# Kernel optimization log

Hardware: AMD Instinct MI355X
Metric: run time of the kernel (lower is better)

## Reference

```python
import jax, jax.numpy as jnp
import numpy as np

EPS = 1e-5  # torch LayerNorm default

def setup_inputs() -> dict:
    key = jax.random.key(0)
    ks = jax.random.split(key, 4)
    S, B, D, BN = 4096, 8, 1024, 128
    x = jax.random.normal(ks[0], (S, B, D), dtype=jnp.float32)
    residual = jax.random.normal(ks[1], (B, S, D), dtype=jnp.float32)
    # xavier_uniform init for adapter projections
    lim_d = float(np.sqrt(6.0 / (D + BN)))
    W_down = jax.random.uniform(ks[2], (BN, D), minval=-lim_d, maxval=lim_d, dtype=jnp.float32)
    W_up = jax.random.uniform(ks[3], (D, BN), minval=-lim_d, maxval=lim_d, dtype=jnp.float32)
    return {
        "x": x,
        "residual": residual,
        "ln_gamma": jnp.ones((D,), jnp.float32),
        "ln_beta": jnp.zeros((D,), jnp.float32),
        "W_down": W_down,
        "b_down": jnp.zeros((BN,), jnp.float32),
        "W_up": W_up,
        "b_up": jnp.zeros((D,), jnp.float32),
    }

def reference(x, residual, ln_gamma, ln_beta, W_down, b_down, W_up, b_up):
    # ffn_fn is an opaque callable (treated as identity here); x: [S,B,D]
    x = x + jnp.swapaxes(residual, 0, 1)           # residual.transpose(0,1)
    shortcut = x
    # NaiveAdapter: LayerNorm -> down -> ReLU -> up -> residual add
    mu = jnp.mean(x, axis=-1, keepdims=True)
    var = jnp.mean(jnp.square(x - mu), axis=-1, keepdims=True)
    h = (x - mu) * jax.lax.rsqrt(var + EPS) * ln_gamma + ln_beta
    h = jax.nn.relu(jnp.einsum('sbd,kd->sbk', h, W_down) + b_down)  # [S,B,BN]
    h = jnp.einsum('sbk,dk->sbd', h, W_up) + b_up                   # [S,B,D]
    return h + shortcut
```

## Files before the change

kernel.cpp:

```cpp
#include <hip/hip_runtime.h>

#define S_DIM 4096
#define B_DIM 8
#define D_DIM 1024
#define BN_DIM 128
#define M_DIM (S_DIM * B_DIM)
#define LDT 40
#define CLD 132

typedef short s8v __attribute__((ext_vector_type(8)));
typedef float f4v __attribute__((ext_vector_type(4)));

__device__ __forceinline__ unsigned short f2bf(float f) {
  union { unsigned int i; float f; } v; v.f = f;
  unsigned int r = v.i + 0x7FFFu + ((v.i >> 16) & 1u);
  return (unsigned short)(r >> 16);
}
__device__ __forceinline__ float bf2f(unsigned short u) {
  union { unsigned int i; float f; } v; v.i = ((unsigned int)u) << 16; return v.f;
}

__global__ __launch_bounds__(256) void prep_kernel(
    const float* __restrict__ Wd_f, const float* __restrict__ bd_f,
    const float* __restrict__ Wu_f, const float* __restrict__ gamma,
    const float* __restrict__ beta,
    unsigned short* __restrict__ Wd, float* __restrict__ bd,
    unsigned short* __restrict__ Wu) {
  __shared__ float red[4];
  int t = threadIdx.x;
  if (blockIdx.x < 128) {
    int n = blockIdx.x, k = t * 4;
    float4 w = *(const float4*)&Wd_f[n * 1024 + k];
    float4 g = *(const float4*)&gamma[k];
    float4 bt = *(const float4*)&beta[k];
    ushort4 o;
    o.x = f2bf(w.x * g.x); o.y = f2bf(w.y * g.y);
    o.z = f2bf(w.z * g.z); o.w = f2bf(w.w * g.w);
    *(ushort4*)&Wd[n * 1024 + k] = o;
    float bs = w.x * bt.x + w.y * bt.y + w.z * bt.z + w.w * bt.w;
#pragma unroll
    for (int ofs = 32; ofs >= 1; ofs >>= 1) bs += __shfl_xor(bs, ofs, 64);
    if ((t & 63) == 0) red[t >> 6] = bs;
    __syncthreads();
    if (t == 0) bd[n] = bd_f[n] + red[0] + red[1] + red[2] + red[3];
  } else {
    int j = blockIdx.x - 128;
#pragma unroll
    for (int c = 0; c < 4; ++c) {
      int idx = j * 4096 + c * 1024 + t * 4;
      float4 w = *(const float4*)&Wu_f[idx];
      ushort4 o;
      o.x = f2bf(w.x); o.y = f2bf(w.y); o.z = f2bf(w.z); o.w = f2bf(w.w);
      *(ushort4*)&Wu[idx] = o;
    }
    __syncthreads();
  }
}

__global__ __launch_bounds__(256) void add_ln_kernel(
    const float* __restrict__ x, const float* __restrict__ res,
    unsigned short* __restrict__ y, float2* __restrict__ stats) {
  int wave = threadIdx.x >> 6, lane = threadIdx.x & 63;
  int row0 = blockIdx.x * 8 + wave * 2;

  float4 xa[2][4], ra[2][4];
#pragma unroll
  for (int p = 0; p < 2; ++p) {
    int row = row0 + p;
    const float* xr = x + (size_t)row * D_DIM;
    const float* rr = res + ((size_t)(row & 7) * S_DIM + (row >> 3)) * D_DIM;
#pragma unroll
    for (int c = 0; c < 4; ++c) {
      int e = c * 256 + lane * 4;
      xa[p][c] = *(const float4*)&xr[e];
      ra[p][c] = *(const float4*)&rr[e];
    }
  }
  float sum[2] = {0.f, 0.f}, sq[2] = {0.f, 0.f};
#pragma unroll
  for (int p = 0; p < 2; ++p)
#pragma unroll
    for (int c = 0; c < 4; ++c) {
      xa[p][c].x += ra[p][c].x; xa[p][c].y += ra[p][c].y;
      xa[p][c].z += ra[p][c].z; xa[p][c].w += ra[p][c].w;
      sum[p] += xa[p][c].x + xa[p][c].y + xa[p][c].z + xa[p][c].w;
      sq[p] += xa[p][c].x * xa[p][c].x + xa[p][c].y * xa[p][c].y +
               xa[p][c].z * xa[p][c].z + xa[p][c].w * xa[p][c].w;
    }
#pragma unroll
  for (int ofs = 32; ofs >= 1; ofs >>= 1) {
    sum[0] += __shfl_xor(sum[0], ofs, 64);
    sq[0]  += __shfl_xor(sq[0], ofs, 64);
    sum[1] += __shfl_xor(sum[1], ofs, 64);
    sq[1]  += __shfl_xor(sq[1], ofs, 64);
  }
#pragma unroll
  for (int p = 0; p < 2; ++p) {
    int row = row0 + p;
    float mu = sum[p] * (1.f / D_DIM);
    float var = sq[p] * (1.f / D_DIM) - mu * mu;
    float rstd = rsqrtf(var + 1e-5f);
    if (lane == 0) stats[row] = make_float2(mu, rstd);
    unsigned short* yr = y + (size_t)row * D_DIM;
#pragma unroll
    for (int c = 0; c < 4; ++c) {
      int e = c * 256 + lane * 4;
      ushort4 o;
      o.x = f2bf(xa[p][c].x); o.y = f2bf(xa[p][c].y);
      o.z = f2bf(xa[p][c].z); o.w = f2bf(xa[p][c].w);
      *(ushort4*)&yr[e] = o;
    }
  }
}

__global__ __launch_bounds__(256) void gemm_down(
    const unsigned short* __restrict__ Y,
    const unsigned short* __restrict__ Wd,
    const float* __restrict__ bd,
    const float2* __restrict__ stats,
    unsigned short* __restrict__ H) {
  __shared__ unsigned short As[64 * LDT];
  __shared__ unsigned short Bs[128 * LDT];
  int t = threadIdx.x, wave = t >> 6, lane = t & 63;
  int tileM = blockIdx.x * 64;
  int arow = t >> 2, akc = (t & 3) * 8;
  float2 st = stats[tileM + arow];
  float rstd = st.y, nmu = -st.x * st.y;

  f4v acc[8];
#pragma unroll
  for (int i = 0; i < 8; ++i) acc[i] = (f4v){0.f, 0.f, 0.f, 0.f};

  for (int kk = 0; kk < 1024; kk += 32) {
    s8v yv = *(const s8v*)&Y[(size_t)(tileM + arow) * 1024 + kk + akc];
    s8v av;
#pragma unroll
    for (int j = 0; j < 8; ++j)
      av[j] = (short)f2bf(bf2f((unsigned short)yv[j]) * rstd + nmu);
    *(s8v*)&As[arow * LDT + akc] = av;
#pragma unroll
    for (int i = 0; i < 2; ++i) {
      int idx = t + i * 256;
      int brow = idx >> 2, bkc = (idx & 3) * 8;
      *(s8v*)&Bs[brow * LDT + bkc] = *(const s8v*)&Wd[(size_t)brow * 1024 + kk + bkc];
    }
    __syncthreads();
    int kq = (lane >> 4) * 8;
    s8v a = *(const s8v*)&As[(wave * 16 + (lane & 15)) * LDT + kq];
#pragma unroll
    for (int nt = 0; nt < 8; ++nt) {
      s8v b = *(const s8v*)&Bs[(nt * 16 + (lane & 15)) * LDT + kq];
      acc[nt] = __builtin_amdgcn_mfma_f32_16x16x32_bf16(a, b, acc[nt], 0, 0, 0);
    }
    __syncthreads();
  }
#pragma unroll
  for (int nt = 0; nt < 8; ++nt) {
    int n = nt * 16 + (lane & 15);
    float bs = bd[n];
#pragma unroll
    for (int r = 0; r < 4; ++r) {
      int m = wave * 16 + (lane >> 4) * 4 + r;
      float val = acc[nt][r] + bs;
      val = val > 0.f ? val : 0.f;
      H[(size_t)(tileM + m) * BN_DIM + n] = f2bf(val);
    }
  }
}

__global__ __launch_bounds__(256) void gemm_up(
    const unsigned short* __restrict__ H,
    const unsigned short* __restrict__ Wu,
    const float* __restrict__ bias,
    const unsigned short* __restrict__ Y,
    float* __restrict__ out) {
  __shared__ unsigned short As[64 * LDT];
  __shared__ unsigned short Bs[128 * LDT];
  __shared__ float Cs[64 * CLD];
  int t = threadIdx.x, wave = t >> 6, lane = t & 63;
  int tileM = blockIdx.x * 64;
  int tileN = blockIdx.y * 128;

  f4v acc[8];
#pragma unroll
  for (int i = 0; i < 8; ++i) acc[i] = (f4v){0.f, 0.f, 0.f, 0.f};

  int arow = t >> 2, akc = (t & 3) * 8;
#pragma unroll
  for (int kk = 0; kk < 128; kk += 32) {
    *(s8v*)&As[arow * LDT + akc] =
        *(const s8v*)&H[(size_t)(tileM + arow) * BN_DIM + kk + akc];
#pragma unroll
    for (int i = 0; i < 2; ++i) {
      int idx = t + i * 256;
      int brow = idx >> 2, bkc = (idx & 3) * 8;
      *(s8v*)&Bs[brow * LDT + bkc] =
          *(const s8v*)&Wu[(size_t)(tileN + brow) * BN_DIM + kk + bkc];
    }
    __syncthreads();
    int kq = (lane >> 4) * 8;
    s8v a = *(const s8v*)&As[(wave * 16 + (lane & 15)) * LDT + kq];
#pragma unroll
    for (int nt = 0; nt < 8; ++nt) {
      s8v b = *(const s8v*)&Bs[(nt * 16 + (lane & 15)) * LDT + kq];
      acc[nt] = __builtin_amdgcn_mfma_f32_16x16x32_bf16(a, b, acc[nt], 0, 0, 0);
    }
    __syncthreads();
  }
#pragma unroll
  for (int nt = 0; nt < 8; ++nt) {
    int nl = nt * 16 + (lane & 15);
    float bs = bias[tileN + nl];
#pragma unroll
    for (int r = 0; r < 4; ++r) {
      int m = wave * 16 + (lane >> 4) * 4 + r;
      Cs[m * CLD + nl] = acc[nt][r] + bs;
    }
  }
  __syncthreads();
#pragma unroll
  for (int pass = 0; pass < 4; ++pass) {
    int m = pass * 16 + (t >> 4);
    int col = (t & 15) * 8;
    size_t gbase = (size_t)(tileM + m) * D_DIM + tileN + col;
    s8v yv = *(const s8v*)&Y[gbase];
    const float* cs = &Cs[m * CLD + col];
    float4 o0, o1;
    o0.x = cs[0] + bf2f((unsigned short)yv[0]);
    o0.y = cs[1] + bf2f((unsigned short)yv[1]);
    o0.z = cs[2] + bf2f((unsigned short)yv[2]);
    o0.w = cs[3] + bf2f((unsigned short)yv[3]);
    o1.x = cs[4] + bf2f((unsigned short)yv[4]);
    o1.y = cs[5] + bf2f((unsigned short)yv[5]);
    o1.z = cs[6] + bf2f((unsigned short)yv[6]);
    o1.w = cs[7] + bf2f((unsigned short)yv[7]);
    *(float4*)&out[gbase] = o0;
    *(float4*)&out[gbase + 4] = o1;
  }
}

extern "C" void kernel_launch(void* const* d_in, const int* in_sizes, int n_in,
                              void* d_out, int out_size, void* d_ws, size_t ws_size,
                              hipStream_t stream) {
  const float* x      = (const float*)d_in[0];
  const float* res    = (const float*)d_in[1];
  const float* gamma  = (const float*)d_in[2];
  const float* beta   = (const float*)d_in[3];
  const float* W_down = (const float*)d_in[4];
  const float* b_down = (const float*)d_in[5];
  const float* W_up   = (const float*)d_in[6];
  const float* b_up   = (const float*)d_in[7];
  float* out = (float*)d_out;

  unsigned short* ws_y  = (unsigned short*)d_ws;
  unsigned short* ws_h1 = ws_y + (size_t)M_DIM * D_DIM;
  float2* ws_stats      = (float2*)(ws_h1 + (size_t)M_DIM * BN_DIM);
  unsigned short* ws_wd = (unsigned short*)(ws_stats + M_DIM);
  float* ws_bd          = (float*)(ws_wd + 128 * 1024);
  unsigned short* ws_wu = (unsigned short*)(ws_bd + 128);

  prep_kernel<<<160, 256, 0, stream>>>(W_down, b_down, W_up, gamma, beta,
                                       ws_wd, ws_bd, ws_wu);
  add_ln_kernel<<<M_DIM / 8, 256, 0, stream>>>(x, res, ws_y, ws_stats);
  gemm_down<<<M_DIM / 64, 256, 0, stream>>>(ws_y, ws_wd, ws_bd, ws_stats, ws_h1);
  gemm_up<<<dim3(M_DIM / 64, D_DIM / 128), 256, 0, stream>>>(ws_h1, ws_wu, b_up,
                                                             ws_y, out);
}
```

Baseline: 415.9 us.

## Restructure all three kernels with register prefetch, double buffering and 2x4 wave tiles

Add_ln becomes a grid-stride loop over one row per wave with a fixed grid of 2048 blocks. gemm_down now uses a K-step of 64, prefetches global tiles into registers, double-buffers shared memory, and assigns each wave a 32x64 output tile so fragments are reused across more MFMAs. gemm_up loads the full K=128 slice in a single stage, reuses the A/B shared buffer for the C staging tile in two passes, and prefetches the Y residual and bias early. Together these aim to cut barrier count and global-latency stalls, at the cost of more registers and shared memory per block, which may lower occupancy.

```diff
diff --git a/kernel.cpp b/kernel.cpp
--- a/kernel.cpp
+++ b/kernel.cpp
@@ -5,7 +5,8 @@
 #define D_DIM 1024
 #define BN_DIM 128
 #define M_DIM (S_DIM * B_DIM)
-#define LDT 40
+#define LDK 72
+#define LDK3 136
 #define CLD 132
 
 typedef short s8v __attribute__((ext_vector_type(8)));
@@ -61,54 +62,39 @@
     const float* __restrict__ x, const float* __restrict__ res,
     unsigned short* __restrict__ y, float2* __restrict__ stats) {
   int wave = threadIdx.x >> 6, lane = threadIdx.x & 63;
-  int row0 = blockIdx.x * 8 + wave * 2;
-
-  float4 xa[2][4], ra[2][4];
-#pragma unroll
-  for (int p = 0; p < 2; ++p) {
-    int row = row0 + p;
+  for (int row = blockIdx.x * 4 + wave; row < M_DIM; row += gridDim.x * 4) {
     const float* xr = x + (size_t)row * D_DIM;
     const float* rr = res + ((size_t)(row & 7) * S_DIM + (row >> 3)) * D_DIM;
+    float4 xa[4], ra[4];
+#pragma unroll
+    for (int c = 0; c < 4; ++c) xa[c] = *(const float4*)&xr[c * 256 + lane * 4];
+#pragma unroll
+    for (int c = 0; c < 4; ++c) ra[c] = *(const float4*)&rr[c * 256 + lane * 4];
+    float sum = 0.f, sq = 0.f;
 #pragma unroll
     for (int c = 0; c < 4; ++c) {
-      int e = c * 256 + lane * 4;
-      xa[p][c] = *(const float4*)&xr[e];
-      ra[p][c] = *(const float4*)&rr[e];
-    }
-  }
-  float sum[2] = {0.f, 0.f}, sq[2] = {0.f, 0.f};
-#pragma unroll
-  for (int p = 0; p < 2; ++p)
-#pragma unroll
-    for (int c = 0; c < 4; ++c) {
-      xa[p][c].x += ra[p][c].x; xa[p][c].y += ra[p][c].y;
-      xa[p][c].z += ra[p][c].z; xa[p][c].w += ra[p][c].w;
-      sum[p] += xa[p][c].x + xa[p][c].y + xa[p][c].z + xa[p][c].w;
-      sq[p] += xa[p][c].x * xa[p][c].x + xa[p][c].y * xa[p][c].y +
-               xa[p][c].z * xa[p][c].z + xa[p][c].w * xa[p][c].w;
-    }
-#pragma unroll
-  for (int ofs = 32; ofs >= 1; ofs >>= 1) {
-    sum[0] += __shfl_xor(sum[0], ofs, 64);
-    sq[0]  += __shfl_xor(sq[0], ofs, 64);
-    sum[1] += __shfl_xor(sum[1], ofs, 64);
-    sq[1]  += __shfl_xor(sq[1], ofs, 64);
-  }
-#pragma unroll
-  for (int p = 0; p < 2; ++p) {
-    int row = row0 + p;
-    float mu = sum[p] * (1.f / D_DIM);
-    float var = sq[p] * (1.f / D_DIM) - mu * mu;
+      xa[c].x += ra[c].x; xa[c].y += ra[c].y;
+      xa[c].z += ra[c].z; xa[c].w += ra[c].w;
+      sum += xa[c].x + xa[c].y + xa[c].z + xa[c].w;
+      sq += xa[c].x * xa[c].x + xa[c].y * xa[c].y +
+            xa[c].z * xa[c].z + xa[c].w * xa[c].w;
+    }
+#pragma unroll
+    for (int ofs = 32; ofs >= 1; ofs >>= 1) {
+      sum += __shfl_xor(sum, ofs, 64);
+      sq  += __shfl_xor(sq, ofs, 64);
+    }
+    float mu = sum * (1.f / D_DIM);
+    float var = sq * (1.f / D_DIM) - mu * mu;
     float rstd = rsqrtf(var + 1e-5f);
     if (lane == 0) stats[row] = make_float2(mu, rstd);
     unsigned short* yr = y + (size_t)row * D_DIM;
 #pragma unroll
     for (int c = 0; c < 4; ++c) {
-      int e = c * 256 + lane * 4;
       ushort4 o;
-      o.x = f2bf(xa[p][c].x); o.y = f2bf(xa[p][c].y);
-      o.z = f2bf(xa[p][c].z); o.w = f2bf(xa[p][c].w);
-      *(ushort4*)&yr[e] = o;
+      o.x = f2bf(xa[c].x); o.y = f2bf(xa[c].y);
+      o.z = f2bf(xa[c].z); o.w = f2bf(xa[c].w);
+      *(ushort4*)&yr[c * 256 + lane * 4] = o;
     }
   }
 }
@@ -119,52 +105,86 @@
     const float* __restrict__ bd,
     const float2* __restrict__ stats,
     unsigned short* __restrict__ H) {
-  __shared__ unsigned short As[64 * LDT];
-  __shared__ unsigned short Bs[128 * LDT];
-  int t = threadIdx.x, wave = t >> 6, lane = t & 63;
+  __shared__ unsigned short sm[2 * (64 * LDK + 128 * LDK)];
+  int t = threadIdx.x, wid = t >> 6, lane = t & 63;
   int tileM = blockIdx.x * 64;
-  int arow = t >> 2, akc = (t & 3) * 8;
+  int arow = t >> 2, ac0 = (t & 3) * 16;
   float2 st = stats[tileM + arow];
   float rstd = st.y, nmu = -st.x * st.y;
-
-  f4v acc[8];
-#pragma unroll
-  for (int i = 0; i < 8; ++i) acc[i] = (f4v){0.f, 0.f, 0.f, 0.f};
-
-  for (int kk = 0; kk < 1024; kk += 32) {
-    s8v yv = *(const s8v*)&Y[(size_t)(tileM + arow) * 1024 + kk + akc];
-    s8v av;
-#pragma unroll
-    for (int j = 0; j < 8; ++j)
-      av[j] = (short)f2bf(bf2f((unsigned short)yv[j]) * rstd + nmu);
-    *(s8v*)&As[arow * LDT + akc] = av;
-#pragma unroll
-    for (int i = 0; i < 2; ++i) {
-      int idx = t + i * 256;
-      int brow = idx >> 2, bkc = (idx & 3) * 8;
-      *(s8v*)&Bs[brow * LDT + bkc] = *(const s8v*)&Wd[(size_t)brow * 1024 + kk + bkc];
-    }
-    __syncthreads();
-    int kq = (lane >> 4) * 8;
-    s8v a = *(const s8v*)&As[(wave * 16 + (lane & 15)) * LDT + kq];
-#pragma unroll
-    for (int nt = 0; nt < 8; ++nt) {
-      s8v b = *(const s8v*)&Bs[(nt * 16 + (lane & 15)) * LDT + kq];
-      acc[nt] = __builtin_amdgcn_mfma_f32_16x16x32_bf16(a, b, acc[nt], 0, 0, 0);
-    }
-    __syncthreads();
-  }
-#pragma unroll
-  for (int nt = 0; nt < 8; ++nt) {
-    int n = nt * 16 + (lane & 15);
+  const unsigned short* Yr = Y + (size_t)(tileM + arow) * D_DIM + ac0;
+  int brow = t >> 1, bc0 = (t & 1) * 32;
+  const unsigned short* Wr = Wd + (size_t)brow * D_DIM + bc0;
+
+  f4v acc[2][4];
+#pragma unroll
+  for (int am = 0; am < 2; ++am)
+#pragma unroll
+    for (int nt = 0; nt < 4; ++nt) acc[am][nt] = (f4v){0.f, 0.f, 0.f, 0.f};
+
+  s8v aR0 = *(const s8v*)&Yr[0], aR1 = *(const s8v*)&Yr[8];
+  s8v bR0 = *(const s8v*)&Wr[0], bR1 = *(const s8v*)&Wr[8];
+  s8v bR2 = *(const s8v*)&Wr[16], bR3 = *(const s8v*)&Wr[24];
+
+  int wm = wid & 1, wn = wid >> 1;
+  int kq = (lane >> 4) * 8, fr = lane & 15;
+  int aoff = arow * LDK + ac0;
+  int boff = 64 * LDK + brow * LDK + bc0;
+
+#pragma unroll 2
+  for (int step = 0; step < 16; ++step) {
+    unsigned short* buf = sm + (step & 1) * (64 * LDK + 128 * LDK);
+    s8v av0, av1;
+#pragma unroll
+    for (int j = 0; j < 8; ++j) {
+      av0[j] = (short)f2bf(bf2f((unsigned short)aR0[j]) * rstd + nmu);
+      av1[j] = (short)f2bf(bf2f((unsigned short)aR1[j]) * rstd + nmu);
+    }
+    *(s8v*)&buf[aoff] = av0;      *(s8v*)&buf[aoff + 8] = av1;
+    *(s8v*)&buf[boff] = bR0;      *(s8v*)&buf[boff + 8] = bR1;
+    *(s8v*)&buf[boff + 16] = bR2; *(s8v*)&buf[boff + 24] = bR3;
+    __syncthreads();
+    if (step < 15) {
+      int kk = (step + 1) * 64;
+      aR0 = *(const s8v*)&Yr[kk];      aR1 = *(const s8v*)&Yr[kk + 8];
+      bR0 = *(const s8v*)&Wr[kk];      bR1 = *(const s8v*)&Wr[kk + 8];
+      bR2 = *(const s8v*)&Wr[kk + 16]; bR3 = *(const s8v*)&Wr[kk + 24];
+    }
+    const unsigned short* As = buf;
+    const unsigned short* Bs = buf + 64 * LDK;
+    s8v a[2][2], b[4][2];
+#pragma unroll
+    for (int am = 0; am < 2; ++am) {
+      const unsigned short* p = &As[(wm * 32 + am * 16 + fr) * LDK + kq];
+      a[am][0] = *(const s8v*)&p[0];
+      a[am][1] = *(const s8v*)&p[32];
+    }
+#pragma unroll
+    for (int nt = 0; nt < 4; ++nt) {
+      const unsigned short* p = &Bs[(wn * 64 + nt * 16 + fr) * LDK + kq];
+      b[nt][0] = *(const s8v*)&p[0];
+      b[nt][1] = *(const s8v*)&p[32];
+    }
+#pragma unroll
+    for (int am = 0; am < 2; ++am)
+#pragma unroll
+      for (int nt = 0; nt < 4; ++nt) {
+        acc[am][nt] = __builtin_amdgcn_mfma_f32_16x16x32_bf16(a[am][0], b[nt][0], acc[am][nt], 0, 0, 0);
+        acc[am][nt] = __builtin_amdgcn_mfma_f32_16x16x32_bf16(a[am][1], b[nt][1], acc[am][nt], 0, 0, 0);
+      }
+  }
+#pragma unroll
+  for (int nt = 0; nt < 4; ++nt) {
+    int n = wn * 64 + nt * 16 + fr;
     float bs = bd[n];
 #pragma unroll
-    for (int r = 0; r < 4; ++r) {
-      int m = wave * 16 + (lane >> 4) * 4 + r;
-      float val = acc[nt][r] + bs;
-      val = val > 0.f ? val : 0.f;
-      H[(size_t)(tileM + m) * BN_DIM + n] = f2bf(val);
-    }
+    for (int am = 0; am < 2; ++am)
+#pragma unroll
+      for (int r = 0; r < 4; ++r) {
+        int m = wm * 32 + am * 16 + (lane >> 4) * 4 + r;
+        float val = acc[am][nt][r] + bs;
+        val = val > 0.f ? val : 0.f;
+        H[(size_t)(tileM + m) * BN_DIM + n] = f2bf(val);
+      }
   }
 }
 
@@ -174,68 +194,92 @@
     const float* __restrict__ bias,
     const unsigned short* __restrict__ Y,
     float* __restrict__ out) {
-  __shared__ unsigned short As[64 * LDT];
-  __shared__ unsigned short Bs[128 * LDT];
-  __shared__ float Cs[64 * CLD];
-  int t = threadIdx.x, wave = t >> 6, lane = t & 63;
-  int tileM = blockIdx.x * 64;
-  int tileN = blockIdx.y * 128;
-
-  f4v acc[8];
-#pragma unroll
-  for (int i = 0; i < 8; ++i) acc[i] = (f4v){0.f, 0.f, 0.f, 0.f};
-
-  int arow = t >> 2, akc = (t & 3) * 8;
-#pragma unroll
-  for (int kk = 0; kk < 128; kk += 32) {
-    *(s8v*)&As[arow * LDT + akc] =
-        *(const s8v*)&H[(size_t)(tileM + arow) * BN_DIM + kk + akc];
-#pragma unroll
-    for (int i = 0; i < 2; ++i) {
-      int idx = t + i * 256;
-      int brow = idx >> 2, bkc = (idx & 3) * 8;
-      *(s8v*)&Bs[brow * LDT + bkc] =
-          *(const s8v*)&Wu[(size_t)(tileN + brow) * BN_DIM + kk + bkc];
-    }
-    __syncthreads();
-    int kq = (lane >> 4) * 8;
-    s8v a = *(const s8v*)&As[(wave * 16 + (lane & 15)) * LDT + kq];
-#pragma unroll
-    for (int nt = 0; nt < 8; ++nt) {
-      s8v b = *(const s8v*)&Bs[(nt * 16 + (lane & 15)) * LDT + kq];
-      acc[nt] = __builtin_amdgcn_mfma_f32_16x16x32_bf16(a, b, acc[nt], 0, 0, 0);
-    }
-    __syncthreads();
-  }
-#pragma unroll
-  for (int nt = 0; nt < 8; ++nt) {
-    int nl = nt * 16 + (lane & 15);
-    float bs = bias[tileN + nl];
-#pragma unroll
-    for (int r = 0; r < 4; ++r) {
-      int m = wave * 16 + (lane >> 4) * 4 + r;
-      Cs[m * CLD + nl] = acc[nt][r] + bs;
-    }
-  }
+  __shared__ __align__(16) unsigned char smraw[(64 + 128) * LDK3 * 2];
+  unsigned short* As = (unsigned short*)smraw;
+  unsigned short* Bs = As + 64 * LDK3;
+  float* Cs = (float*)smraw;
+  int t = threadIdx.x, wid = t >> 6, lane = t & 63;
+  int tileM = blockIdx.x * 64, tileN = blockIdx.y * BN_DIM;
+
+#pragma unroll
+  for (int i = 0; i < 4; ++i) {
+    int ch = i * 256 + t, r = ch >> 4, c = (ch & 15) * 8;
+    *(s8v*)&As[r * LDK3 + c] = *(const s8v*)&H[(size_t)(tileM + r) * BN_DIM + c];
+  }
+#pragma unroll
+  for (int i = 0; i < 8; ++i) {
+    int ch = i * 256 + t, r = ch >> 4, c = (ch & 15) * 8;
+    *(s8v*)&Bs[r * LDK3 + c] = *(const s8v*)&Wu[(size_t)(tileN + r) * BN_DIM + c];
+  }
+  int erow = t >> 4, ecol = (t & 15) * 8;
+  s8v yv[4];
+#pragma unroll
+  for (int p = 0; p < 4; ++p)
+    yv[p] = *(const s8v*)&Y[(size_t)(tileM + p * 16 + erow) * D_DIM + tileN + ecol];
+  float4 bv0 = *(const float4*)&bias[tileN + ecol];
+  float4 bv1 = *(const float4*)&bias[tileN + ecol + 4];
   __syncthreads();
-#pragma unroll
-  for (int pass = 0; pass < 4; ++pass) {
-    int m = pass * 16 + (t >> 4);
-    int col = (t & 15) * 8;
-    size_t gbase = (size_t)(tileM + m) * D_DIM + tileN + col;
-    s8v yv = *(const s8v*)&Y[gbase];
-    const float* cs = &Cs[m * CLD + col];
-    float4 o0, o1;
-    o0.x = cs[0] + bf2f((unsigned short)yv[0]);
-    o0.y = cs[1] + bf2f((unsigned short)yv[1]);
-    o0.z = cs[2] + bf2f((unsigned short)yv[2]);
-    o0.w = cs[3] + bf2f((unsigned short)yv[3]);
-    o1.x = cs[4] + bf2f((unsigned short)yv[4]);
-    o1.y = cs[5] + bf2f((unsigned short)yv[5]);
-    o1.z = cs[6] + bf2f((unsigned short)yv[6]);
-    o1.w = cs[7] + bf2f((unsigned short)yv[7]);
-    *(float4*)&out[gbase] = o0;
-    *(float4*)&out[gbase + 4] = o1;
+
+  int wm = wid & 1, wn = wid >> 1, kq = (lane >> 4) * 8, fr = lane & 15;
+  f4v acc[2][4];
+#pragma unroll
+  for (int am = 0; am < 2; ++am)
+#pragma unroll
+    for (int nt = 0; nt < 4; ++nt) acc[am][nt] = (f4v){0.f, 0.f, 0.f, 0.f};
+
+  s8v a[2][4];
+#pragma unroll
+  for (int am = 0; am < 2; ++am) {
+    const unsigned short* p = &As[(wm * 32 + am * 16 + fr) * LDK3 + kq];
+#pragma unroll
+    for (int ks = 0; ks < 4; ++ks) a[am][ks] = *(const s8v*)&p[ks * 32];
+  }
+#pragma unroll
+  for (int nt = 0; nt < 4; ++nt) {
+    const unsigned short* p = &Bs[(wn * 64 + nt * 16 + fr) * LDK3 + kq];
+#pragma unroll
+    for (int ks = 0; ks < 4; ++ks) {
+      s8v b = *(const s8v*)&p[ks * 32];
+#pragma unroll
+      for (int am = 0; am < 2; ++am)
+        acc[am][nt] = __builtin_amdgcn_mfma_f32_16x16x32_bf16(a[am][ks], b, acc[am][nt], 0, 0, 0);
+    }
+  }
+#pragma unroll
+  for (int pass = 0; pass < 2; ++pass) {
+    __syncthreads();
+    if (wm == pass) {
+#pragma unroll
+      for (int nt = 0; nt < 4; ++nt) {
+        int n = wn * 64 + nt * 16 + fr;
+#pragma unroll
+        for (int am = 0; am < 2; ++am)
+#pragma unroll
+          for (int r = 0; r < 4; ++r) {
+            int ml = am * 16 + (lane >> 4) * 4 + r;
+            Cs[ml * CLD + n] = acc[am][nt][r];
+          }
+      }
+    }
+    __syncthreads();
+#pragma unroll
+    for (int s = 0; s < 2; ++s) {
+      int ml = s * 16 + erow;
+      size_t gbase = (size_t)(tileM + pass * 32 + ml) * D_DIM + tileN + ecol;
+      const float* cs = &Cs[ml * CLD + ecol];
+      s8v yq = yv[pass * 2 + s];
+      float4 o0, o1;
+      o0.x = cs[0] + bv0.x + bf2f((unsigned short)yq[0]);
+      o0.y = cs[1] + bv0.y + bf2f((unsigned short)yq[1]);
+      o0.z = cs[2] + bv0.z + bf2f((unsigned short)yq[2]);
+      o0.w = cs[3] + bv0.w + bf2f((unsigned short)yq[3]);
+      o1.x = cs[4] + bv1.x + bf2f((unsigned short)yq[4]);
+      o1.y = cs[5] + bv1.y + bf2f((unsigned short)yq[5]);
+      o1.z = cs[6] + bv1.z + bf2f((unsigned short)yq[6]);
+      o1.w = cs[7] + bv1.w + bf2f((unsigned short)yq[7]);
+      *(float4*)&out[gbase] = o0;
+      *(float4*)&out[gbase + 4] = o1;
+    }
   }
 }
 
@@ -261,7 +305,7 @@
 
   prep_kernel<<<160, 256, 0, stream>>>(W_down, b_down, W_up, gamma, beta,
                                        ws_wd, ws_bd, ws_wu);
-  add_ln_kernel<<<M_DIM / 8, 256, 0, stream>>>(x, res, ws_y, ws_stats);
+  add_ln_kernel<<<2048, 256, 0, stream>>>(x, res, ws_y, ws_stats);
   gemm_down<<<M_DIM / 64, 256, 0, stream>>>(ws_y, ws_wd, ws_bd, ws_stats, ws_h1);
   gemm_up<<<dim3(M_DIM / 64, D_DIM / 128), 256, 0, stream>>>(ws_h1, ws_wu, b_up,
                                                              ws_y, out);
```

Measured after the change: 401.9 us. 1.03x faster.
